# Kernel tuning notes

Hardware: AMD Instinct MI355X
Metric: run time of the kernel (lower is better)

Reference implementation:

```python
import jax, jax.numpy as jnp
import numpy as np

HIDDEN = 64

def setup_inputs() -> dict:
    key = jax.random.key(0)
    ks = jax.random.split(key, 9)
    B, C, H, W = 32, 64, 64, 64
    h = HIDDEN
    s = 0.05
    return {
        "inputs": jax.random.normal(ks[0], (B, C, H, W), jnp.float32),
        # 1x1 Conv2d input->4h gates, stored as [4h, C]
        "w_i2s": jax.random.normal(ks[1], (4 * h, C), jnp.float32) * s,
        "b_i2s": jax.random.normal(ks[2], (4 * h,), jnp.float32) * s,
        # Conv1d(h, 4h, kernel=2): [4h, h, 2]
        "w_s2s": jax.random.normal(ks[3], (4 * h, h, 2), jnp.float32) * s,
        "b_s2s": jax.random.normal(ks[4], (4 * h,), jnp.float32) * s,
        # Conv1d(h, h, kernel=2): [h, h, 2]
        "w_c2c": jax.random.normal(ks[5], (h, h, 2), jnp.float32) * s,
        "b_c2c": jax.random.normal(ks[6], (h,), jnp.float32) * s,
        # 1x1 Conv2d h->2h upsampling, stored as [2h, h]
        "w_up": jax.random.normal(ks[7], (2 * h, h), jnp.float32) * s,
        "b_up": jax.random.normal(ks[8], (2 * h,), jnp.float32) * s,
    }


def _diagonal_lstm(inputs, w_i2s, b_i2s, w_s2s, b_s2s, w_c2c, b_c2c, w_up, b_up):
    B, C, H, W = inputs.shape
    h = w_s2s.shape[1]
    NW = H + W - 1  # skewed width

    # ---- skew: row r of the image shifted right by r columns ----
    rows = jnp.arange(H)[:, None]          # [H,1]
    cols = rows + jnp.arange(W)[None, :]   # [H,W]
    skewed = jnp.zeros((B, C, H, NW), inputs.dtype).at[:, :, rows, cols].set(inputs)

    # ---- input-to-state 1x1 conv -> [B, 4h, H, NW] ----
    i2s = jnp.einsum('bchw,oc->bohw', skewed, w_i2s) + b_i2s[None, :, None, None]
    # per-step input: [NW, B, H*4h]  (layout (H, 4h) flattened, as in torch)
    rnn_in = jnp.transpose(i2s, (3, 0, 2, 1)).reshape(NW, B, H * 4 * h)

    # conv1d(kernel=2) taps: out[p] = W0 @ state[p-1] + W1 @ state[p] (+bias)
    Ws0, Ws1 = w_s2s[:, :, 0], w_s2s[:, :, 1]
    Wc0, Wc1 = w_c2c[:, :, 0], w_c2c[:, :, 1]

    def step(carry, i2s_t):
        c_prev, h_prev = carry  # each [B, H, h]
        zrow = jnp.zeros((B, 1, h), inputs.dtype)
        h_shift = jnp.concatenate([zrow, h_prev[:, :-1]], axis=1)
        c_shift = jnp.concatenate([zrow, c_prev[:, :-1]], axis=1)
        s2s = (jnp.einsum('bph,oh->bpo', h_shift, Ws0)
               + jnp.einsum('bph,oh->bpo', h_prev, Ws1)
               + b_s2s)                       # [B, H, 4h]
        c2c = (jnp.einsum('bph,oh->bpo', c_shift, Wc0)
               + jnp.einsum('bph,oh->bpo', c_prev, Wc1)
               + b_c2c)                       # [B, H, h]
        lstm = jax.nn.sigmoid(i2s_t + s2s.reshape(B, H * 4 * h))
        ig, gg, fg, og = jnp.split(lstm, 4, axis=1)  # each [B, h*H] (faithful flat split)
        c2c_flat = c2c.reshape(B, H * h)
        c = fg * c2c_flat + ig * gg
        hh = og * jnp.tanh(c)
        new_carry = (c.reshape(B, H, h), hh.reshape(B, H, h))
        return new_carry, hh

    init = (jnp.zeros((B, H, h), inputs.dtype), jnp.zeros((B, H, h), inputs.dtype))
    _, outs = jax.lax.scan(step, init, rnn_in)   # outs: [NW, B, H*h]

    # [NW,B,H*h] -> [B, NW, H, h] -> [B, h, H, NW]
    outs = jnp.transpose(outs, (1, 0, 2)).reshape(B, NW, H, h)
    skewed_out = jnp.transpose(outs, (0, 3, 2, 1))

    # ---- unskew ----
    unskewed = skewed_out[:, :, rows, cols]  # [B, h, H, W]

    # ---- 1x1 upsampling conv h -> 2h ----
    return jnp.einsum('bchw,oc->bohw', unskewed, w_up) + b_up[None, :, None, None]


def reference(inputs, w_i2s, b_i2s, w_s2s, b_s2s, w_c2c, b_c2c, w_up, b_up):
    return _diagonal_lstm(inputs, w_i2s, b_i2s, w_s2s, b_s2s, w_c2c, b_c2c, w_up, b_up)
```

## Files before the change

### kernel.cpp

```cpp
#include <hip/hip_runtime.h>
#include <cstdint>
#include <cstddef>


typedef unsigned int u32;
typedef unsigned short u16;
typedef __bf16 bf16x8 __attribute__((ext_vector_type(8)));
typedef float f32x4 __attribute__((ext_vector_type(4)));

#define NSTEP 127
#define MFMA(a, b, c) __builtin_amdgcn_mfma_f32_16x16x32_bf16(a, b, c, 0, 0, 0)
#define LOG2E 1.4426950408889634f
#define SCL (-1.4426950408889634f)
#define T2L 2.8853900817779268f
#define RHO(r) ((((r) ^ ((r) >> 3))) & 7)

static __device__ __forceinline__ u16 f2bf(float f) {
    u32 u = __builtin_bit_cast(u32, f);
    u32 r = u + 0x7FFFu + ((u >> 16) & 1u);
    return (u16)(r >> 16);
}
static __device__ __forceinline__ u32 pack2(float a, float b) {
    return (u32)f2bf(a) | ((u32)f2bf(b) << 16);
}
static __device__ __forceinline__ float lo2f(u32 u) {
    return __builtin_bit_cast(float, u << 16);
}
static __device__ __forceinline__ float hi2f(u32 u) {
    return __builtin_bit_cast(float, u & 0xFFFF0000u);
}
static __device__ __forceinline__ float sigm2(float y) {
    return __builtin_amdgcn_rcpf(1.f + __builtin_amdgcn_exp2f(y));
}
static __device__ __forceinline__ float tanh_fast(float x) {
    float r = __builtin_amdgcn_rcpf(1.f + __builtin_amdgcn_exp2f(x * T2L));
    return __builtin_fmaf(-2.f, r, 1.f);
}

__global__ __launch_bounds__(256) void repack_w(
    const float* __restrict__ w_s2s, const float* __restrict__ w_c2c,
    const float* __restrict__ bi, const float* __restrict__ bs,
    const float* __restrict__ w_up, float* __restrict__ Wg,
    float* __restrict__ Wc, u16* __restrict__ biasRow,
    u16* __restrict__ w_upB) {
    int idx = blockIdx.x * 256 + threadIdx.x;
    if (idx < 32768) {
        int o = idx >> 7, kk = idx & 127, half = kk >> 6, k = kk & 63;
        Wg[idx] = SCL * w_s2s[(o * 64 + k) * 2 + half];
        return;
    }
    int j = idx - 32768;
    if (j < 8192) {
        int o = j >> 7, kk = j & 127, half = kk >> 6, k = kk & 63;
        Wc[j] = w_c2c[(o * 64 + k) * 2 + half];
        return;
    }
    j -= 8192;
    if (j < 256) {
        int m15 = j >> 4, nq = (j >> 2) & 3, nb = j & 3;
        int o = 64 * nq + 16 * nb + m15;
        biasRow[j] = f2bf(SCL * (bi[o] + bs[o]));
        return;
    }
    j -= 256;
    if (j < 8192) w_upB[j] = f2bf(w_up[j]);
}

__global__ __launch_bounds__(256, 2) void i2s_kernel(
    const float* __restrict__ in, const float* __restrict__ w_i2s,
    const float* __restrict__ bi, const float* __restrict__ bs,
    const u32* __restrict__ biasU32, u32* __restrict__ out_u32) {
    const int bid = blockIdx.x;
    const int b = bid >> 6, r = bid & 63;
    const int tid = threadIdx.x;
    const int lane = tid & 63;
    const int wv = __builtin_amdgcn_readfirstlane(tid >> 6);
    const int m15 = lane & 15, g4 = lane >> 4;

    __shared__ __align__(16) u32 sT[64 * 129];
    __shared__ __align__(16) u32 Xt[64 * 32];
    char* XtB = (char*)Xt;

    {
        const int w = tid & 63, cp = tid >> 6;
        const float* xp = in + (size_t)b * 262144 + r * 64 + w;
#pragma unroll
        for (int pass = 0; pass < 8; pass++) {
            int c = pass * 8 + cp * 2;
            float x0 = xp[(size_t)c * 4096];
            float x1 = xp[(size_t)(c + 1) * 4096];
            *(u32*)(XtB + ((w * 128 + c * 2) ^ ((w & 7) << 4))) = pack2(x0, x1);
        }
    }

    bf16x8 Af[4][2];
#pragma unroll
    for (int m = 0; m < 4; m++)
#pragma unroll
        for (int kt = 0; kt < 2; kt++) {
            const float* p =
                w_i2s + (wv * 64 + m * 16 + m15) * 64 + kt * 32 + g4 * 8;
            bf16x8 f;
#pragma unroll
            for (int j = 0; j < 8; j++) f[j] = (__bf16)p[j];
            Af[m][kt] = f;
        }
    float bias[4][4];
#pragma unroll
    for (int m = 0; m < 4; m++)
#pragma unroll
        for (int reg = 0; reg < 4; reg++) {
            int o = wv * 64 + m * 16 + 4 * g4 + reg;
            bias[m][reg] = bi[o] + bs[o];
        }

    __syncthreads();

    f32x4 acc[4][4] = {};
#pragma unroll
    for (int nt = 0; nt < 4; nt++) {
        const int w = nt * 16 + m15;
        bf16x8 Bf[2];
#pragma unroll
        for (int kt = 0; kt < 2; kt++)
            Bf[kt] = __builtin_bit_cast(
                bf16x8, *(const uint4*)(XtB + ((w * 128 + kt * 64 + g4 * 16) ^
                                               ((w & 7) << 4))));
#pragma unroll
        for (int m = 0; m < 4; m++)
#pragma unroll
            for (int kt = 0; kt < 2; kt++)
                acc[m][nt] = MFMA(Af[m][kt], Bf[kt], acc[m][nt]);
    }

#pragma unroll
    for (int nt = 0; nt < 4; nt++) {
        const int w = nt * 16 + m15;
#pragma unroll
        for (int reg = 0; reg < 4; reg++)
#pragma unroll
            for (int mp = 0; mp < 2; mp++) {
                float v0 = SCL * (acc[2 * mp][nt][reg] + bias[2 * mp][reg]);
                float v1 =
                    SCL * (acc[2 * mp + 1][nt][reg] + bias[2 * mp + 1][reg]);
                sT[w * 129 + (4 * g4 + reg) * 8 + wv * 2 + mp] = pack2(v0, v1);
            }
    }
    __syncthreads();

    const size_t base = ((size_t)(b * 64 + r) * 66 + 1) * 128;
#pragma unroll
    for (int loop = 0; loop < 32; loop++) {
        int idx = loop * 256 + tid;
        int w = idx >> 7, cu = idx & 127;
        out_u32[base + idx] = sT[w * 129 + cu];
    }
    if (tid < 128) {
        u32 v = biasU32[tid];
        out_u32[base - 128 + tid] = v;
        out_u32[base + 8192 + tid] = v;
    }
}

__global__ __launch_bounds__(512, 2) void scan_kernel(
    const u16* __restrict__ i2sP, const float* __restrict__ Wg,
    const float* __restrict__ Wc, const float* __restrict__ b_c2c,
    u16* __restrict__ hh16) {
    const int b = blockIdx.x;
    const int tid = threadIdx.x;
    const int lane = tid & 63;
    const int wv = __builtin_amdgcn_readfirstlane(tid >> 6);
    const int mh = wv >> 2, nq = wv & 3;
    const int mtc = wv >> 1, ktc0 = (wv & 1) * 2;
    const int m15 = lane & 15, g4 = lane >> 4;

    __shared__ __align__(16) u32 sM[10304];
    __shared__ __align__(16) u32 sCCm[2048];
    char* smB = (char*)sM;
    char* ccB = (char*)sCCm;

    for (int i = tid; i < 10304; i += 512) sM[i] = 0;

    bf16x8 BW[4][4];
    float bcc[4];
#pragma unroll
    for (int nb = 0; nb < 4; nb++) {
        int o = 64 * nq + 16 * nb + m15;
        bcc[nb] = b_c2c[16 * nb + m15];
#pragma unroll
        for (int kt = 0; kt < 4; kt++) {
            const float* p = Wg + o * 128 + kt * 32 + g4 * 8;
            bf16x8 f;
#pragma unroll
            for (int j = 0; j < 8; j++) f[j] = (__bf16)p[j];
            BW[nb][kt] = f;
        }
    }
    bf16x8 BC[2][4];
#pragma unroll
    for (int i = 0; i < 2; i++) {
        int o2 = 16 * (ktc0 + i) + m15;
#pragma unroll
        for (int kt = 0; kt < 4; kt++) {
            const float* p = Wc + o2 * 128 + kt * 32 + g4 * 8;
            bf16x8 f;
#pragma unroll
            for (int j = 0; j < 8; j++) f[j] = (__bf16)p[j];
            BC[i][kt] = f;
        }
    }

    int aG[2][4], aC[4], wOff[2][4], ccR[2][4], ccP[4], bOffB[2][4];
#pragma unroll
    for (int mi = 0; mi < 2; mi++) {
        int mt = 2 * mh + mi;
#pragma unroll
        for (int kt = 0; kt < 4; kt++) {
            int P = 16 * (m15 & 3) + 4 * mt + (m15 >> 2);
            int phys = P + (kt >> 1) - 1;
            int chunk = (kt & 1) * 4 + g4;
            aG[mi][kt] = (phys < 0) ? (32768 + chunk * 16)
                                    : (phys * 128 + ((chunk ^ RHO(phys)) * 16));
        }
        int p2 = 16 * mt + 4 * g4 + nq;
#pragma unroll
        for (int nb = 0; nb < 4; nb++) {
            int k = 16 * nb + m15;
            wOff[mi][nb] =
                8192 + p2 * 128 + (((k >> 3) ^ RHO(p2)) * 16) + (k & 7) * 2;
            int rp = p2 >> 1;
            ccR[mi][nb] = (rp * 64 + ((k + 8 * rp) & 63)) * 4;
            int prerow = 16 * nb + 4 * mt + g4;
            bOffB[mi][nb] = (prerow * 66 + 1) * 512 + 32 * m15 + 8 * nq;
        }
    }
#pragma unroll
    for (int kt = 0; kt < 4; kt++) {
        int crow = 16 * mtc + m15;
        int phys = crow + (kt >> 1) - 1;
        int chunk = (kt & 1) * 4 + g4;
        aC[kt] = (phys < 0) ? (32896 + chunk * 16)
                            : (16384 + phys * 128 + ((chunk ^ RHO(phys)) * 16));
    }
#pragma unroll
    for (int i = 0; i < 2; i++) {
        int k = 16 * (ktc0 + i) + m15;
        int rp0 = 8 * mtc + 2 * g4, rp1 = rp0 + 1;
        ccP[2 * i] = (rp0 * 64 + ((k + 8 * rp0) & 63)) * 4;
        ccP[2 * i + 1] = (rp1 * 64 + ((k + 8 * rp1) & 63)) * 4;
    }

    const char* i2sB = (const char*)i2sP + (size_t)b * (64 * 66 * 512);
    u16* hp16[2];
    int p2s[2];
#pragma unroll
    for (int mi = 0; mi < 2; mi++) {
        int p2 = 16 * (2 * mh + mi) + 4 * g4 + nq;
        p2s[mi] = p2;
        hp16[mi] = hh16 + (size_t)b * 262144 + p2 * 4032 + m15;
    }

    __syncthreads();

    for (int t = 0; t < NSTEP; t++) {
        uint2 IV[2][4];
#pragma unroll
        for (int mi = 0; mi < 2; mi++) {
            int mt = 2 * mh + mi;
#pragma unroll
            for (int r = 0; r < 4; r++) {
                int prerow = 16 * r + 4 * mt + g4;
                int w = min(max(t - prerow, -1), 64);
                IV[mi][r] =
                    *(const uint2*)(i2sB + (bOffB[mi][r] + (w << 9)));
            }
        }

        f32x4 accG[2][4] = {};
#pragma unroll
        for (int mi = 0; mi < 2; mi++) {
            bf16x8 Ag[4];
#pragma unroll
            for (int kt = 0; kt < 4; kt++)
                Ag[kt] = __builtin_bit_cast(bf16x8,
                                            *(const uint4*)(smB + aG[mi][kt]));
#pragma unroll
            for (int nb = 0; nb < 4; nb++)
#pragma unroll
                for (int kt = 0; kt < 4; kt++)
                    accG[mi][nb] = MFMA(Ag[kt], BW[nb][kt], accG[mi][nb]);
        }
        f32x4 accC[2] = {};
        {
            bf16x8 Ac[4];
#pragma unroll
            for (int kt = 0; kt < 4; kt++)
                Ac[kt] =
                    __builtin_bit_cast(bf16x8, *(const uint4*)(smB + aC[kt]));
#pragma unroll
            for (int i = 0; i < 2; i++)
#pragma unroll
                for (int kt = 0; kt < 4; kt++)
                    accC[i] = MFMA(Ac[kt], BC[i][kt], accC[i]);
        }

#pragma unroll
        for (int mi = 0; mi < 2; mi++)
#pragma unroll
            for (int r = 0; r < 4; r++) {
                u32 w0 = IV[mi][r].x, w1 = IV[mi][r].y;
                accG[mi][0][r] += lo2f(w0);
                accG[mi][1][r] += hi2f(w0);
                accG[mi][2][r] += lo2f(w1);
                accG[mi][3][r] += hi2f(w1);
            }

#pragma unroll
        for (int i = 0; i < 2; i++) {
            *(u32*)(ccB + ccP[2 * i]) = pack2(accC[i][0], accC[i][1]);
            *(u32*)(ccB + ccP[2 * i + 1]) = pack2(accC[i][2], accC[i][3]);
        }
        __syncthreads();

#pragma unroll
        for (int mi = 0; mi < 2; mi++) {
            int p2 = p2s[mi];
            bool vst = (u32)(t - p2) < 64u;
            u16* hp = hp16[mi];
#pragma unroll
            for (int nb = 0; nb < 4; nb++) {
                u32 cw = *(const u32*)(ccB + ccR[mi][nb]);
                float cc = ((nq & 1) ? hi2f(cw) : lo2f(cw)) + bcc[nb];
                float si = sigm2(accG[mi][nb][0]);
                float sg = sigm2(accG[mi][nb][1]);
                float sf = sigm2(accG[mi][nb][2]);
                float so = sigm2(accG[mi][nb][3]);
                float c1 = __builtin_fmaf(sf, cc, si * sg);
                float h1 = so * tanh_fast(c1);
                u16 hb = f2bf(h1);
                *(u16*)(smB + wOff[mi][nb]) = hb;
                *(u16*)(smB + wOff[mi][nb] + 16384) = f2bf(c1);
                if (vst) hp[nb * 16] = hb;
            }
            hp16[mi] += 64;
        }
        __syncthreads();

#pragma unroll
        for (int mi = 0; mi < 2; mi++) {
#pragma unroll
            for (int kt = 0; kt < 4; kt++) aG[mi][kt] ^= 8192;
#pragma unroll
            for (int nb = 0; nb < 4; nb++) wOff[mi][nb] ^= 8192;
        }
#pragma unroll
        for (int kt = 0; kt < 4; kt++) aC[kt] ^= 8192;
    }
}

__global__ __launch_bounds__(256) void up_kernel(
    const u16* __restrict__ hh16, const u16* __restrict__ w_upB,
    const float* __restrict__ b_up, float* __restrict__ out) {
    const int bid = blockIdx.x;
    const int b = bid >> 6, r = bid & 63;
    const int lane = threadIdx.x & 63;
    const int wt = __builtin_amdgcn_readfirstlane(threadIdx.x >> 6);
    const int m15 = lane & 15, g4 = lane >> 4;

    const u16* hh_b = hh16 + (size_t)b * 262144;
    const int w = 16 * wt + m15;

    bf16x8 Bf[2];
#pragma unroll
    for (int kt = 0; kt < 2; kt++)
        Bf[kt] = __builtin_bit_cast(
            bf16x8,
            *(const uint4*)(hh_b + (r * 4096 + w * 64 + kt * 32 + g4 * 8)));

    f32x4 acc[8] = {};
#pragma unroll
    for (int nt = 0; nt < 8; nt++) {
#pragma unroll
        for (int kt = 0; kt < 2; kt++) {
            bf16x8 Af = __builtin_bit_cast(
                bf16x8, *(const uint4*)(w_upB + ((16 * nt + m15) * 64 +
                                                 kt * 32 + g4 * 8)));
            acc[nt] = MFMA(Af, Bf[kt], acc[nt]);
        }
    }
    float* outb = out + (size_t)b * 524288;
#pragma unroll
    for (int nt = 0; nt < 8; nt++) {
#pragma unroll
        for (int rr = 0; rr < 4; rr++) {
            int o2 = 16 * nt + 4 * g4 + rr;
            outb[(size_t)o2 * 4096 + r * 64 + w] = acc[nt][rr] + b_up[o2];
        }
    }
}

extern "C" void kernel_launch(void* const* d_in, const int* in_sizes, int n_in,
                              void* d_out, int out_size, void* d_ws,
                              size_t ws_size, hipStream_t stream) {
    (void)in_sizes; (void)n_in; (void)out_size; (void)ws_size;
    const float* inputs = (const float*)d_in[0];
    const float* w_i2s = (const float*)d_in[1];
    const float* b_i2s = (const float*)d_in[2];
    const float* w_s2s = (const float*)d_in[3];
    const float* b_s2s = (const float*)d_in[4];
    const float* w_c2c = (const float*)d_in[5];
    const float* b_c2c = (const float*)d_in[6];
    const float* w_up = (const float*)d_in[7];
    const float* b_up = (const float*)d_in[8];
    float* out = (float*)d_out;
    char* ws = (char*)d_ws;

    u16* i2sP = (u16*)ws;
    u16* hh16 = (u16*)(ws + 69206016);
    float* Wg = (float*)(ws + 85983232);
    float* Wc = (float*)(ws + 86114304);
    u16* biasRow = (u16*)(ws + 86147072);
    u16* w_upB = (u16*)(ws + 86147584);

    hipLaunchKernelGGL(repack_w, dim3(193), dim3(256), 0, stream, w_s2s, w_c2c,
                       b_i2s, b_s2s, w_up, Wg, Wc, biasRow, w_upB);
    hipLaunchKernelGGL(i2s_kernel, dim3(2048), dim3(256), 0, stream, inputs,
                       w_i2s, b_i2s, b_s2s, (const u32*)biasRow, (u32*)i2sP);
    hipLaunchKernelGGL(scan_kernel, dim3(32), dim3(512), 0, stream, i2sP, Wg,
                       Wc, b_c2c, hh16);
    hipLaunchKernelGGL(up_kernel, dim3(2048), dim3(256), 0, stream, hh16,
                       w_upB, b_up, out);
}
```

Before: 495.9 us.

## Prefetch next-step i2s inputs and defer global h stores in LSTM scan

The recurrent loop now loads the i2s gate inputs for step t+1 while computing step t, so the global-memory latency sits off the critical path of the serial recurrence. Accumulators are seeded with the prefetched inputs instead of adding them after the MFMAs. The global write of h is postponed to the start of the next iteration so the store does not sit between the two barriers. This costs extra registers for the prefetched and held values and could reduce occupancy or cause spills.

```diff
diff --git a/kernel.cpp b/kernel.cpp
--- a/kernel.cpp
+++ b/kernel.cpp
@@ -260,25 +260,60 @@
         hp16[mi] = hh16 + (size_t)b * 262144 + p2 * 4032 + m15;
     }
 
+    uint2 IV[2][4];
+#pragma unroll
+    for (int mi = 0; mi < 2; mi++) {
+        int mt = 2 * mh + mi;
+#pragma unroll
+        for (int r = 0; r < 4; r++) {
+            int prerow = 16 * r + 4 * mt + g4;
+            int w = min(max(0 - prerow, -1), 64);
+            IV[mi][r] = *(const uint2*)(i2sB + (bOffB[mi][r] + (w << 9)));
+        }
+    }
+
+    u16 hbKeep[2][4];
+    u16* hpPrev[2];
+    bool vstPrev[2];
+#pragma unroll
+    for (int mi = 0; mi < 2; mi++) {
+        vstPrev[mi] = false;
+        hpPrev[mi] = hp16[mi];
+    }
+
     __syncthreads();
 
     for (int t = 0; t < NSTEP; t++) {
-        uint2 IV[2][4];
+#pragma unroll
+        for (int mi = 0; mi < 2; mi++)
+            if (vstPrev[mi]) {
+#pragma unroll
+                for (int nb = 0; nb < 4; nb++)
+                    hpPrev[mi][nb * 16] = hbKeep[mi][nb];
+            }
+
+        uint2 IVn[2][4];
 #pragma unroll
         for (int mi = 0; mi < 2; mi++) {
             int mt = 2 * mh + mi;
 #pragma unroll
             for (int r = 0; r < 4; r++) {
                 int prerow = 16 * r + 4 * mt + g4;
-                int w = min(max(t - prerow, -1), 64);
-                IV[mi][r] =
-                    *(const uint2*)(i2sB + (bOffB[mi][r] + (w << 9)));
+                int w = min(max(t + 1 - prerow, -1), 64);
+                IVn[mi][r] = *(const uint2*)(i2sB + (bOffB[mi][r] + (w << 9)));
             }
         }
 
-        f32x4 accG[2][4] = {};
+        f32x4 accG[2][4];
 #pragma unroll
         for (int mi = 0; mi < 2; mi++) {
+#pragma unroll
+            for (int r = 0; r < 4; r++) {
+                accG[mi][0][r] = lo2f(IV[mi][r].x);
+                accG[mi][1][r] = hi2f(IV[mi][r].x);
+                accG[mi][2][r] = lo2f(IV[mi][r].y);
+                accG[mi][3][r] = hi2f(IV[mi][r].y);
+            }
             bf16x8 Ag[4];
 #pragma unroll
             for (int kt = 0; kt < 4; kt++)
@@ -305,17 +340,6 @@
         }
 
 #pragma unroll
-        for (int mi = 0; mi < 2; mi++)
-#pragma unroll
-            for (int r = 0; r < 4; r++) {
-                u32 w0 = IV[mi][r].x, w1 = IV[mi][r].y;
-                accG[mi][0][r] += lo2f(w0);
-                accG[mi][1][r] += hi2f(w0);
-                accG[mi][2][r] += lo2f(w1);
-                accG[mi][3][r] += hi2f(w1);
-            }
-
-#pragma unroll
         for (int i = 0; i < 2; i++) {
             *(u32*)(ccB + ccP[2 * i]) = pack2(accC[i][0], accC[i][1]);
             *(u32*)(ccB + ccP[2 * i + 1]) = pack2(accC[i][2], accC[i][3]);
@@ -326,7 +350,6 @@
         for (int mi = 0; mi < 2; mi++) {
             int p2 = p2s[mi];
             bool vst = (u32)(t - p2) < 64u;
-            u16* hp = hp16[mi];
 #pragma unroll
             for (int nb = 0; nb < 4; nb++) {
                 u32 cw = *(const u32*)(ccB + ccR[mi][nb]);
@@ -340,8 +363,10 @@
                 u16 hb = f2bf(h1);
                 *(u16*)(smB + wOff[mi][nb]) = hb;
                 *(u16*)(smB + wOff[mi][nb] + 16384) = f2bf(c1);
-                if (vst) hp[nb * 16] = hb;
+                hbKeep[mi][nb] = hb;
             }
+            vstPrev[mi] = vst;
+            hpPrev[mi] = hp16[mi];
             hp16[mi] += 64;
         }
         __syncthreads();
@@ -349,6 +374,8 @@
 #pragma unroll
         for (int mi = 0; mi < 2; mi++) {
 #pragma unroll
+            for (int r = 0; r < 4; r++) IV[mi][r] = IVn[mi][r];
+#pragma unroll
             for (int kt = 0; kt < 4; kt++) aG[mi][kt] ^= 8192;
 #pragma unroll
             for (int nb = 0; nb < 4; nb++) wOff[mi][nb] ^= 8192;
@@ -356,6 +383,14 @@
 #pragma unroll
         for (int kt = 0; kt < 4; kt++) aC[kt] ^= 8192;
     }
+
+#pragma unroll
+    for (int mi = 0; mi < 2; mi++)
+        if (vstPrev[mi]) {
+#pragma unroll
+            for (int nb = 0; nb < 4; nb++)
+                hpPrev[mi][nb * 16] = hbKeep[mi][nb];
+        }
 }
 
 __global__ __launch_bounds__(256) void up_kernel(
```

Result: faster. 444.7 us (-10.3%).
